# Kernel tuning notes

Hardware: AMD Instinct MI355X
Metric: run time of the kernel (lower is better)

The kernel has to match this reference:

```python
import jax, jax.numpy as jnp
import numpy as np

N_NODES = 50000
N_EDGES = 800000
IN_DIM = 128
HID = 32
HEADS = 4


def _lin_init(key, fan_in, fan_out):
    k1, k2 = jax.random.split(key)
    s = 1.0 / np.sqrt(fan_in)
    W = jax.random.uniform(k1, (fan_in, fan_out), jnp.float32, -s, s)
    b = jax.random.uniform(k2, (fan_out,), jnp.float32, -s, s)
    return W, b


def setup_inputs() -> dict:
    key = jax.random.key(0)
    keys = jax.random.split(key, 12)
    x = jax.random.normal(keys[0], (N_NODES, IN_DIM), jnp.float32)
    edge_index = jax.random.randint(keys[1], (2, N_EDGES), 0, N_NODES, jnp.int64)

    # conv1: in_dim -> heads*hid (128 -> 4*32)
    Wq1, bq1 = _lin_init(keys[2], IN_DIM, HEADS * HID)
    Wk1, bk1 = _lin_init(keys[3], IN_DIM, HEADS * HID)
    Wv1, bv1 = _lin_init(keys[4], IN_DIM, HEADS * HID)
    Ws1, bs1 = _lin_init(keys[5], IN_DIM, HEADS * HID)
    # conv2: 128 -> 1*32
    Wq2, bq2 = _lin_init(keys[6], HEADS * HID, HID)
    Wk2, bk2 = _lin_init(keys[7], HEADS * HID, HID)
    Wv2, bv2 = _lin_init(keys[8], HEADS * HID, HID)
    Ws2, bs2 = _lin_init(keys[9], HEADS * HID, HID)
    # output linear: 32 -> 1
    Wo, bo = _lin_init(keys[10], HID, 1)

    return {
        "x": x, "edge_index": edge_index,
        "Wq1": Wq1, "bq1": bq1, "Wk1": Wk1, "bk1": bk1,
        "Wv1": Wv1, "bv1": bv1, "Ws1": Ws1, "bs1": bs1,
        "Wq2": Wq2, "bq2": bq2, "Wk2": Wk2, "bk2": bk2,
        "Wv2": Wv2, "bv2": bv2, "Ws2": Ws2, "bs2": bs2,
        "Wo": Wo, "bo": bo,
    }


def transformer_conv(x, edge_index, Wq, bq, Wk, bk, Wv, bv, Ws, bs, heads, d):
    # PyG TransformerConv (concat=True, root_weight=True, beta=False, no edge attr).
    n = x.shape[0]
    src, dst = edge_index[0], edge_index[1]  # message j(src) -> i(dst)
    q = (x @ Wq + bq).reshape(n, heads, d)
    k = (x @ Wk + bk).reshape(n, heads, d)
    v = (x @ Wv + bv).reshape(n, heads, d)
    # per-edge attention logits [E, heads]
    logits = (q[dst] * k[src]).sum(-1) / jnp.sqrt(jnp.float32(d))
    # segment softmax over incoming edges of each target node
    m = jax.ops.segment_max(logits, dst, num_segments=n)
    p = jnp.exp(logits - m[dst])
    denom = jax.ops.segment_sum(p, dst, num_segments=n)
    alpha = p / denom[dst]  # [E, heads]
    # weighted scatter-add of values
    msg = alpha[:, :, None] * v[src]  # [E, heads, d]
    aggr = jax.ops.segment_sum(msg, dst, num_segments=n).reshape(n, heads * d)
    return aggr + x @ Ws + bs  # root (skip) connection


def reference(x, edge_index,
              Wq1, bq1, Wk1, bk1, Wv1, bv1, Ws1, bs1,
              Wq2, bq2, Wk2, bk2, Wv2, bv2, Ws2, bs2,
              Wo, bo):
    h = transformer_conv(x, edge_index, Wq1, bq1, Wk1, bk1, Wv1, bv1, Ws1, bs1, HEADS, HID)
    h = jax.nn.relu(h)
    h = transformer_conv(h, edge_index, Wq2, bq2, Wk2, bk2, Wv2, bv2, Ws2, bs2, 1, HID)
    h = jax.nn.relu(h)
    g = h.mean(axis=0)  # [HID]
    return g @ Wo + bo  # [1]
```

## Files before the change

### kernel.cpp

```cpp
#include <hip/hip_runtime.h>
#include <math.h>

#define N_NODES 50000
#define N_EDGES 800000
#define NBK 196
#define BCAP 6144

typedef short short8 __attribute__((ext_vector_type(8)));
typedef float f32x4 __attribute__((ext_vector_type(4)));
typedef float f32x2 __attribute__((ext_vector_type(2)));

__device__ inline unsigned short f2bf(float v) {
  unsigned u = __float_as_uint(v);
  u += 0x7FFFu + ((u >> 16) & 1u);
  return (unsigned short)(u >> 16);
}
__device__ inline float bf2f(unsigned short b) {
  return __uint_as_float(((unsigned)b) << 16);
}
__device__ inline float bflo(unsigned u) { return __uint_as_float(u << 16); }
__device__ inline float bfhi(unsigned u) { return __uint_as_float(u & 0xFFFF0000u); }
__device__ inline unsigned char f2fp8(float v) {
  return (unsigned char)(__builtin_amdgcn_cvt_pk_fp8_f32(v, 0.f, 0, false) & 0xFF);
}
template <bool HI>
__device__ inline f32x2 fp8dec(unsigned u) {
  return __builtin_amdgcn_cvt_pk_f32_fp8(u, HI);
}

#define SCL 0.17677669529663687f

#define CAST_B 6250
#define C1_B 256
#define C2_B 64
__global__ void prep_fused(const float* __restrict__ x,
                           const float* __restrict__ Wq1, const float* __restrict__ Wk1,
                           const float* __restrict__ Wv1, const float* __restrict__ Ws1,
                           const float* __restrict__ bq1, const float* __restrict__ bk1,
                           const float* __restrict__ bv1, const float* __restrict__ bs1,
                           const float* __restrict__ Wq2, const float* __restrict__ Wk2,
                           const float* __restrict__ Wv2, const float* __restrict__ Ws2,
                           const float* __restrict__ bq2, const float* __restrict__ bk2,
                           const float* __restrict__ bv2, const float* __restrict__ bs2,
                           unsigned short* __restrict__ xb, unsigned short* __restrict__ Wt1,
                           float* __restrict__ bcat1, unsigned short* __restrict__ Wt2,
                           float* __restrict__ bcat2, int* __restrict__ bhist,
                           float* __restrict__ ACC) {
  const int b = blockIdx.x, tid = threadIdx.x;
  if (b < CAST_B) {
    int i = b * 256 + tid;
    float4 v = ((const float4*)x)[i];
    ushort4 o;
    o.x = f2bf(v.x); o.y = f2bf(v.y); o.z = f2bf(v.z); o.w = f2bf(v.w);
    ((ushort4*)xb)[i] = o;
  } else if (b < CAST_B + C1_B) {
    int i = (b - CAST_B) * 256 + tid;
    int c = i >> 7, k = i & 127;
    int mi = c >> 7, lc = c & 127;
    const float* W = (mi == 0) ? Wq1 : (mi == 1) ? Wk1 : (mi == 2) ? Wv1 : Ws1;
    float scl = (mi == 0) ? SCL : 1.f;
    Wt1[i] = f2bf(W[(size_t)k * 128 + lc] * scl);
    if (i < 512) {
      int bm = i >> 7, bl = i & 127;
      const float* bb = (bm == 0) ? bq1 : (bm == 1) ? bk1 : (bm == 2) ? bv1 : bs1;
      bcat1[i] = bb[bl] * ((bm == 0) ? SCL : 1.f);
    }
  } else if (b < CAST_B + C1_B + C2_B) {
    int i = (b - CAST_B - C1_B) * 256 + tid;
    int c = i >> 7, k = i & 127;
    int mi = c >> 5, lc = c & 31;
    const float* W = (mi == 0) ? Wq2 : (mi == 1) ? Wk2 : (mi == 2) ? Wv2 : Ws2;
    float scl = (mi == 0) ? SCL : 1.f;
    Wt2[i] = f2bf(W[(size_t)k * 32 + lc] * scl);
    if (i < 128) {
      int bm = i >> 5, bl = i & 31;
      const float* bb = (bm == 0) ? bq2 : (bm == 1) ? bk2 : (bm == 2) ? bv2 : bs2;
      bcat2[i] = bb[bl] * ((bm == 0) ? SCL : 1.f);
    }
  } else {
    if (tid < NBK) bhist[tid] = 0;
    else if (tid >= 224 && tid < 256) ACC[tid - 224] = 0.f;
  }
}

__global__ __launch_bounds__(256) void gemm_conv1(
    const unsigned short* __restrict__ Ab, const unsigned short* __restrict__ Wt,
    const float* __restrict__ bcat, unsigned short* __restrict__ Q1b,
    unsigned short* __restrict__ SK1, unsigned char* __restrict__ KV8, int M) {
  __shared__ __align__(16) unsigned char L[3][64 * 272];
  unsigned short* As = (unsigned short*)L[0];
  const int bm = blockIdx.x * 64;
  const int tid = threadIdx.x, wave = tid >> 6, lane = tid & 63;
  const int lr = lane & 15, q = lane >> 4;

#pragma unroll
  for (int p = 0; p < 4; ++p) {
    int f = tid + p * 256;
    int row = f >> 4, chunk = f & 15;
    int gm = bm + row; if (gm >= M) gm = 0;
    uint4 v = *(const uint4*)(Ab + (size_t)gm * 128 + chunk * 8);
    *(uint4*)&As[row * 136 + chunk * 8] = v;
  }
  __syncthreads();

  const int colbase = wave * 128;
  f32x4 acc[4][8];
#pragma unroll
  for (int i = 0; i < 4; ++i)
#pragma unroll
    for (int j = 0; j < 8; ++j) acc[i][j] = (f32x4){0.f, 0.f, 0.f, 0.f};

#pragma unroll
  for (int ks = 0; ks < 4; ++ks) {
    short8 af[4];
#pragma unroll
    for (int i = 0; i < 4; ++i)
      af[i] = *(short8*)&As[(i * 16 + lr) * 136 + ks * 32 + q * 8];
#pragma unroll
    for (int j = 0; j < 8; ++j) {
      short8 bf = *(const short8*)(Wt + (size_t)(colbase + j * 16 + lr) * 128 + ks * 32 + q * 8);
#pragma unroll
      for (int i = 0; i < 4; ++i)
        acc[i][j] = __builtin_amdgcn_mfma_f32_16x16x32_bf16(af[i], bf, acc[i][j], 0, 0, 0);
    }
  }
  __syncthreads();

  float bj[8];
#pragma unroll
  for (int j = 0; j < 8; ++j) bj[j] = bcat[colbase + j * 16 + lr];

  if (wave == 0 || wave == 3) {
    unsigned short* Ls16 = (unsigned short*)((wave == 0) ? L[1] : L[0]);
#pragma unroll
    for (int i = 0; i < 4; ++i)
#pragma unroll
      for (int r = 0; r < 4; ++r) {
        int row = i * 16 + q * 4 + r;
#pragma unroll
        for (int j = 0; j < 8; ++j)
          Ls16[row * 136 + j * 16 + lr] = f2bf(acc[i][j][r] + bj[j]);
      }
  } else {
    unsigned char* KLs = L[2];
    const int voff = (wave == 2) ? 2 : 0;
#pragma unroll
    for (int i = 0; i < 4; ++i)
#pragma unroll
      for (int r = 0; r < 4; ++r) {
        int row = i * 16 + q * 4 + r;
#pragma unroll
        for (int j = 0; j < 8; ++j) {
          int d = j * 16 + lr;
          KLs[row * 272 + 4 * (d >> 1) + voff + (d & 1)] = f2fp8(acc[i][j][r] + bj[j]);
        }
      }
  }
  __syncthreads();

#pragma unroll
  for (int p = 0; p < 4; ++p) {
    int f = tid + p * 256;
    int row = f >> 4, u = f & 15;
    int gr = bm + row;
    if (gr < M) {
      *(uint4*)(Q1b + (size_t)gr * 128 + u * 8) = *(uint4*)&((unsigned short*)L[1])[row * 136 + u * 8];
      *(uint4*)(KV8 + (size_t)gr * 256 + u * 16) = *(uint4*)&L[2][row * 272 + u * 16];
      *(uint4*)(SK1 + (size_t)gr * 128 + u * 8) = *(uint4*)&((unsigned short*)L[0])[row * 136 + u * 8];
    }
  }
}

__global__ __launch_bounds__(256) void gemm2(
    const unsigned short* __restrict__ Ab, const unsigned short* __restrict__ Wt,
    const float* __restrict__ bcat, unsigned char* __restrict__ C2b, int M) {
  __shared__ __align__(16) unsigned short As[64 * 136];
  __shared__ __align__(16) unsigned char Lsb[64 * 272];
  const int bm = blockIdx.x * 64;
  const int tid = threadIdx.x, wave = tid >> 6, lane = tid & 63;
  const int lr = lane & 15, q = lane >> 4;

#pragma unroll
  for (int p = 0; p < 4; ++p) {
    int f = tid + p * 256;
    int row = f >> 4, chunk = f & 15;
    int gm = bm + row; if (gm >= M) gm = 0;
    uint4 v = *(const uint4*)(Ab + (size_t)gm * 128 + chunk * 8);
    *(uint4*)&As[row * 136 + chunk * 8] = v;
  }
  __syncthreads();

  f32x4 acc[4][2];
#pragma unroll
  for (int i = 0; i < 4; ++i)
#pragma unroll
    for (int j = 0; j < 2; ++j) acc[i][j] = (f32x4){0.f, 0.f, 0.f, 0.f};

#pragma unroll
  for (int ks = 0; ks < 4; ++ks) {
    short8 af[4];
#pragma unroll
    for (int i = 0; i < 4; ++i)
      af[i] = *(short8*)&As[(i * 16 + lr) * 136 + ks * 32 + q * 8];
#pragma unroll
    for (int j = 0; j < 2; ++j) {
      short8 bf = *(const short8*)(Wt + (size_t)(wave * 32 + j * 16 + lr) * 128 + ks * 32 + q * 8);
#pragma unroll
      for (int i = 0; i < 4; ++i)
        acc[i][j] = __builtin_amdgcn_mfma_f32_16x16x32_bf16(af[i], bf, acc[i][j], 0, 0, 0);
    }
  }

  float bj[2];
#pragma unroll
  for (int j = 0; j < 2; ++j) bj[j] = bcat[wave * 32 + j * 16 + lr];
#pragma unroll
  for (int i = 0; i < 4; ++i)
#pragma unroll
    for (int r = 0; r < 4; ++r) {
      int row = i * 16 + q * 4 + r;
#pragma unroll
      for (int j = 0; j < 2; ++j) {
        int c = wave * 32 + j * 16 + lr;
        float val = acc[i][j][r] + bj[j];
        if (c < 32) {
          *(unsigned short*)&Lsb[row * 272 + 2 * c] = f2bf(val);
        } else if (c < 64) {
          int d = c - 32;
          Lsb[row * 272 + 64 + 4 * (d >> 1) + (d & 1)] = f2fp8(val);
        } else if (c < 96) {
          int d = c - 64;
          Lsb[row * 272 + 64 + 4 * (d >> 1) + 2 + (d & 1)] = f2fp8(val);
        } else {
          *(unsigned short*)&Lsb[row * 272 + 192 + 2 * (c - 96)] = f2bf(val);
        }
      }
    }
  __syncthreads();
#pragma unroll
  for (int p = 0; p < 16; ++p) {
    int idx = tid + p * 256;
    int row = idx >> 6, u = idx & 63;
    int gr = bm + row;
    if (gr < M) *(unsigned*)(C2b + (size_t)gr * 256 + u * 4) = *(const unsigned*)&Lsb[row * 272 + u * 4];
  }
}

__global__ void bucket_hist(const int* __restrict__ ei, int* __restrict__ bhist, int E) {
  __shared__ int h[NBK];
  for (int i = threadIdx.x; i < NBK; i += 256) h[i] = 0;
  __syncthreads();
  int e = blockIdx.x * 4096 + threadIdx.x;
#pragma unroll
  for (int p = 0; p < 16; ++p, e += 256)
    if (e < E) atomicAdd(&h[ei[E + e] >> 8], 1);
  __syncthreads();
  for (int i = threadIdx.x; i < NBK; i += 256)
    if (h[i]) atomicAdd(&bhist[i], h[i]);
}

__global__ void bucket_scan(const int* __restrict__ bhist, int* __restrict__ boff,
                            int* __restrict__ bcur) {
  __shared__ int s[256];
  int t = threadIdx.x;
  int v = (t < NBK) ? bhist[t] : 0;
  s[t] = v;
  __syncthreads();
#pragma unroll
  for (int off = 1; off < 256; off <<= 1) {
    int u = (t >= off) ? s[t - off] : 0;
    __syncthreads();
    s[t] += u;
    __syncthreads();
  }
  if (t < NBK) {
    int excl = s[t] - v;
    boff[t] = excl;
    bcur[t] = excl;
  }
  if (t == NBK - 1) boff[NBK] = s[t];
}

__global__ void bucket_scatter(const int* __restrict__ ei, int* __restrict__ bcur,
                               int2* __restrict__ ebuck, int E) {
  __shared__ int lh[NBK];
  for (int i = threadIdx.x; i < NBK; i += 256) lh[i] = 0;
  __syncthreads();
  const int e0 = blockIdx.x * 4096;
  int srcs[16], dsts[16];
#pragma unroll
  for (int p = 0; p < 16; ++p) {
    int e = e0 + p * 256 + threadIdx.x;
    if (e < E) {
      srcs[p] = ei[e];
      dsts[p] = ei[E + e];
      atomicAdd(&lh[dsts[p] >> 8], 1);
    } else dsts[p] = -1;
  }
  __syncthreads();
  for (int i = threadIdx.x; i < NBK; i += 256)
    if (lh[i]) lh[i] = atomicAdd(&bcur[i], lh[i]);
  __syncthreads();
#pragma unroll
  for (int p = 0; p < 16; ++p) {
    if (dsts[p] >= 0) {
      int slot = atomicAdd(&lh[dsts[p] >> 8], 1);
      ebuck[slot] = make_int2(srcs[p], dsts[p]);
    }
  }
}

__global__ void bucket_csr(const int2* __restrict__ ebuck, const int* __restrict__ boff,
                           int* __restrict__ rowptr, int* __restrict__ esrc, int N) {
  const int b = blockIdx.x;
  const int lo = boff[b], hi = boff[b + 1];
  const int cnt = hi - lo;
  __shared__ int hist[256];
  __shared__ int cur[256];
  __shared__ int sorted[BCAP];
  const int t = threadIdx.x;
  hist[t] = 0;
  __syncthreads();
  for (int i = t; i < cnt; i += 256) {
    int2 ed = ebuck[lo + i];
    atomicAdd(&hist[ed.y & 255], 1);
  }
  __syncthreads();
  int v = hist[t];
  sorted[t] = v;
  __syncthreads();
#pragma unroll
  for (int off = 1; off < 256; off <<= 1) {
    int u = (t >= off) ? sorted[t - off] : 0;
    __syncthreads();
    sorted[t] += u;
    __syncthreads();
  }
  int excl = sorted[t] - v;
  cur[t] = excl;
  int node = b * 256 + t;
  if (node <= N) rowptr[node] = lo + excl;
  __syncthreads();
  for (int i = t; i < cnt; i += 256) {
    int2 ed = ebuck[lo + i];
    int slot = atomicAdd(&cur[ed.y & 255], 1);
    if (slot < BCAP) sorted[slot] = ed.x;
    else esrc[lo + slot] = ed.x << 8;
  }
  __syncthreads();
  int lim = cnt < BCAP ? cnt : BCAP;
  for (int i = t; i < lim; i += 256) esrc[lo + i] = sorted[i] << 8;
}

__global__ void node_attn1(const int* __restrict__ rowptr, const int* __restrict__ esrc,
                           const unsigned short* __restrict__ Qb,
                           const unsigned char* __restrict__ KV8,
                           const unsigned short* __restrict__ SK, unsigned short* __restrict__ Hb,
                           int n) {
  int node = (blockIdx.x * blockDim.x + threadIdx.x) >> 6;
  int lane = threadIdx.x & 63;
  if (node >= n) return;
  const int half = lane >> 5, ll = lane & 31;
  const int r0 = rowptr[node], r1 = rowptr[node + 1];
  uint2 qq = *(const uint2*)(Qb + (size_t)node * 128 + ll * 4);
  const float q0 = bflo(qq.x), q1 = bfhi(qq.x), q2 = bflo(qq.y), q3 = bfhi(qq.y);
  float l = 0.f, a0 = 0.f, a1 = 0.f, a2 = 0.f, a3 = 0.f;
  const unsigned char* kvb = KV8 + ll * 8;
  int j = r0;
  for (; j + 8 <= r1; j += 8) {
    int e = j + half * 4;
    int s0 = esrc[e], s1 = esrc[e + 1], s2 = esrc[e + 2], s3 = esrc[e + 3];
    uint2 u0 = *(const uint2*)(kvb + s0);
    uint2 u1 = *(const uint2*)(kvb + s1);
    uint2 u2 = *(const uint2*)(kvb + s2);
    uint2 u3 = *(const uint2*)(kvb + s3);
    f32x2 k0a = fp8dec<false>(u0.x), k0b = fp8dec<false>(u0.y);
    f32x2 k1a = fp8dec<false>(u1.x), k1b = fp8dec<false>(u1.y);
    f32x2 k2a = fp8dec<false>(u2.x), k2b = fp8dec<false>(u2.y);
    f32x2 k3a = fp8dec<false>(u3.x), k3b = fp8dec<false>(u3.y);
    float d0 = q0 * k0a.x + q1 * k0a.y + q2 * k0b.x + q3 * k0b.y;
    float d1 = q0 * k1a.x + q1 * k1a.y + q2 * k1b.x + q3 * k1b.y;
    float d2 = q0 * k2a.x + q1 * k2a.y + q2 * k2b.x + q3 * k2b.y;
    float d3 = q0 * k3a.x + q1 * k3a.y + q2 * k3b.x + q3 * k3b.y;
#pragma unroll
    for (int msk = 1; msk <= 4; msk <<= 1) {
      d0 += __shfl_xor(d0, msk);
      d1 += __shfl_xor(d1, msk);
      d2 += __shfl_xor(d2, msk);
      d3 += __shfl_xor(d3, msk);
    }
    float p0 = __expf(d0), p1 = __expf(d1), p2 = __expf(d2), p3 = __expf(d3);
    l += (p0 + p1) + (p2 + p3);
    f32x2 v0a = fp8dec<true>(u0.x), v0b = fp8dec<true>(u0.y);
    f32x2 v1a = fp8dec<true>(u1.x), v1b = fp8dec<true>(u1.y);
    f32x2 v2a = fp8dec<true>(u2.x), v2b = fp8dec<true>(u2.y);
    f32x2 v3a = fp8dec<true>(u3.x), v3b = fp8dec<true>(u3.y);
    a0 += p0 * v0a.x + p1 * v1a.x + p2 * v2a.x + p3 * v3a.x;
    a1 += p0 * v0a.y + p1 * v1a.y + p2 * v2a.y + p3 * v3a.y;
    a2 += p0 * v0b.x + p1 * v1b.x + p2 * v2b.x + p3 * v3b.x;
    a3 += p0 * v0b.y + p1 * v1b.y + p2 * v2b.y + p3 * v3b.y;
  }
  for (; j < r1; j += 4) {
    int eA = j + half * 2, eB = eA + 1;
    bool vA = eA < r1, vB = eB < r1;
    int sA = esrc[vA ? eA : r0];
    int sB = esrc[vB ? eB : r0];
    uint2 ua = *(const uint2*)(kvb + sA);
    uint2 ub = *(const uint2*)(kvb + sB);
    f32x2 ka1 = fp8dec<false>(ua.x), ka2 = fp8dec<false>(ua.y);
    f32x2 kb1 = fp8dec<false>(ub.x), kb2 = fp8dec<false>(ub.y);
    float dA = q0 * ka1.x + q1 * ka1.y + q2 * ka2.x + q3 * ka2.y;
    float dB = q0 * kb1.x + q1 * kb1.y + q2 * kb2.x + q3 * kb2.y;
#pragma unroll
    for (int msk = 1; msk <= 4; msk <<= 1) {
      dA += __shfl_xor(dA, msk);
      dB += __shfl_xor(dB, msk);
    }
    float pA = vA ? __expf(dA) : 0.f;
    float pB = vB ? __expf(dB) : 0.f;
    l += pA + pB;
    f32x2 va1 = fp8dec<true>(ua.x), va2 = fp8dec<true>(ua.y);
    f32x2 vb1 = fp8dec<true>(ub.x), vb2 = fp8dec<true>(ub.y);
    a0 += pA * va1.x + pB * vb1.x;
    a1 += pA * va1.y + pB * vb1.y;
    a2 += pA * va2.x + pB * vb2.x;
    a3 += pA * va2.y + pB * vb2.y;
  }
  l  += __shfl_xor(l, 32);
  a0 += __shfl_xor(a0, 32);
  a1 += __shfl_xor(a1, 32);
  a2 += __shfl_xor(a2, 32);
  a3 += __shfl_xor(a3, 32);
  float inv = (l > 0.f) ? 1.f / l : 0.f;
  if (half == 0) {
    uint2 sk = *(const uint2*)(SK + (size_t)node * 128 + ll * 4);
    float o0 = fmaxf(bflo(sk.x) + a0 * inv, 0.f);
    float o1 = fmaxf(bfhi(sk.x) + a1 * inv, 0.f);
    float o2 = fmaxf(bflo(sk.y) + a2 * inv, 0.f);
    float o3 = fmaxf(bfhi(sk.y) + a3 * inv, 0.f);
    uint2 hb;
    hb.x = ((unsigned)f2bf(o1) << 16) | (unsigned)f2bf(o0);
    hb.y = ((unsigned)f2bf(o3) << 16) | (unsigned)f2bf(o2);
    *(uint2*)(Hb + (size_t)node * 128 + ll * 4) = hb;
  }
}

__global__ void node_attn2(const int* __restrict__ rowptr, const int* __restrict__ esrc,
                           unsigned char* __restrict__ C2b, int n) {
  int node = (blockIdx.x * blockDim.x + threadIdx.x) >> 6;
  int lane = threadIdx.x & 63;
  if (node >= n) return;
  const int g = lane >> 4, gl = lane & 15;
  const int r0 = rowptr[node], r1 = rowptr[node + 1];
  unsigned qu = *(const unsigned*)(C2b + (size_t)node * 256 + gl * 4);
  const float q0 = bflo(qu), q1 = bfhi(qu);
  float l = 0.f, a0 = 0.f, a1 = 0.f;
  const unsigned char* kvb = C2b + 64 + gl * 4;
  int j = r0;
  for (; j + 8 <= r1; j += 8) {
    int e = j + g * 2;
    int s0 = esrc[e], s1 = esrc[e + 1];
    unsigned u0 = *(const unsigned*)(kvb + s0);
    unsigned u1 = *(const unsigned*)(kvb + s1);
    f32x2 k0 = fp8dec<false>(u0), k1 = fp8dec<false>(u1);
    float d0 = q0 * k0.x + q1 * k0.y;
    float d1 = q0 * k1.x + q1 * k1.y;
#pragma unroll
    for (int msk = 1; msk <= 8; msk <<= 1) {
      d0 += __shfl_xor(d0, msk);
      d1 += __shfl_xor(d1, msk);
    }
    float p0 = __expf(d0), p1 = __expf(d1);
    l += p0 + p1;
    f32x2 v0 = fp8dec<true>(u0), v1 = fp8dec<true>(u1);
    a0 += p0 * v0.x + p1 * v1.x;
    a1 += p0 * v0.y + p1 * v1.y;
  }
  for (; j < r1; j += 4) {
    bool v = (j + g) < r1;
    int s = esrc[v ? j + g : r0];
    unsigned u = *(const unsigned*)(kvb + s);
    f32x2 kd = fp8dec<false>(u);
    float d = q0 * kd.x + q1 * kd.y;
#pragma unroll
    for (int msk = 1; msk <= 8; msk <<= 1) d += __shfl_xor(d, msk);
    float p = v ? __expf(d) : 0.f;
    l += p;
    f32x2 vd = fp8dec<true>(u);
    a0 += p * vd.x;
    a1 += p * vd.y;
  }
#pragma unroll
  for (int msk = 16; msk <= 32; msk <<= 1) {
    l  += __shfl_xor(l, msk);
    a0 += __shfl_xor(a0, msk);
    a1 += __shfl_xor(a1, msk);
  }
  float inv = (l > 0.f) ? 1.f / l : 0.f;
  if (lane < 16) {
    unsigned* h = (unsigned*)(C2b + (size_t)node * 256 + 192 + gl * 4);
    unsigned hu = *h;
    float o0 = bflo(hu) + a0 * inv;
    float o1 = bfhi(hu) + a1 * inv;
    *h = ((unsigned)f2bf(o1) << 16) | (unsigned)f2bf(o0);
  }
}

__global__ void mean_reduce(const unsigned char* __restrict__ C2b, float* __restrict__ ACC, int n) {
  __shared__ float s[256];
  float acc = 0.f;
  int stride = gridDim.x * blockDim.x;
  int total = n * 32;
  for (int i = blockIdx.x * blockDim.x + threadIdx.x; i < total; i += stride) {
    int node = i >> 5, c = i & 31;
    unsigned short h = *(const unsigned short*)(C2b + (size_t)node * 256 + 192 + c * 2);
    acc += fmaxf(bf2f(h), 0.f);
  }
  s[threadIdx.x] = acc;
  __syncthreads();
  for (int off = 128; off >= 32; off >>= 1) {
    if (threadIdx.x < off) s[threadIdx.x] += s[threadIdx.x + off];
    __syncthreads();
  }
  if (threadIdx.x < 32) atomicAdd(&ACC[threadIdx.x], s[threadIdx.x]);
}

__global__ void final_out(const float* __restrict__ ACC, const float* __restrict__ Wo,
                          const float* __restrict__ bo, float* __restrict__ out, float invN) {
  int lane = threadIdx.x;
  float v = 0.f;
  if (lane < 32) v = ACC[lane] * invN * Wo[lane];
  v += __shfl_xor(v, 1);
  v += __shfl_xor(v, 2);
  v += __shfl_xor(v, 4);
  v += __shfl_xor(v, 8);
  v += __shfl_xor(v, 16);
  v += __shfl_xor(v, 32);
  if (lane == 0) out[0] = v + bo[0];
}

extern "C" void kernel_launch(void* const* d_in, const int* in_sizes, int n_in,
                              void* d_out, int out_size, void* d_ws, size_t ws_size,
                              hipStream_t stream) {
  const float* x   = (const float*)d_in[0];
  const int*   ei  = (const int*)d_in[1];
  const float* Wq1 = (const float*)d_in[2];  const float* bq1 = (const float*)d_in[3];
  const float* Wk1 = (const float*)d_in[4];  const float* bk1 = (const float*)d_in[5];
  const float* Wv1 = (const float*)d_in[6];  const float* bv1 = (const float*)d_in[7];
  const float* Ws1 = (const float*)d_in[8];  const float* bs1 = (const float*)d_in[9];
  const float* Wq2 = (const float*)d_in[10]; const float* bq2 = (const float*)d_in[11];
  const float* Wk2 = (const float*)d_in[12]; const float* bk2 = (const float*)d_in[13];
  const float* Wv2 = (const float*)d_in[14]; const float* bv2 = (const float*)d_in[15];
  const float* Ws2 = (const float*)d_in[16]; const float* bs2 = (const float*)d_in[17];
  const float* Wo  = (const float*)d_in[18]; const float* bo  = (const float*)d_in[19];

  char* ws = (char*)d_ws;
  const int N = N_NODES, E = N_EDGES;
  const int GB = (N + 63) / 64;
  const int EB = (E + 4095) / 4096;

  unsigned short* xb  = (unsigned short*)(ws + 0);
  unsigned short* Q1b = (unsigned short*)(ws + 12800000);
  unsigned short* SK1 = (unsigned short*)(ws + 25600000);
  unsigned char*  KV1 = (unsigned char*)(ws + 38400000);
  unsigned short* H1b = (unsigned short*)(ws + 64000000);
  unsigned char*  C2  = (unsigned char*)(ws + 76800000);
  int* rowptr = (int*)(ws + 102400000);
  int* esrc   = (int*)(ws + 102700032);
  int* bhist  = (int*)(ws + 105900032);
  int* boff   = (int*)(ws + 105901056);
  int* bcur   = (int*)(ws + 105902080);
  unsigned short* Wt1   = (unsigned short*)(ws + 105903104);
  unsigned short* Wt2   = (unsigned short*)(ws + 106034176);
  float*          bcat1 = (float*)(ws + 106066944);
  float*          bcat2 = (float*)(ws + 106068992);
  float*          ACC   = (float*)(ws + 106069504);
  int2*           ebuck = (int2*)(ws + 106070016);

  float* out = (float*)d_out;

  dim3 blk(256);

  prep_fused<<<dim3(CAST_B + C1_B + C2_B + 1), blk, 0, stream>>>(
      x, Wq1, Wk1, Wv1, Ws1, bq1, bk1, bv1, bs1,
      Wq2, Wk2, Wv2, Ws2, bq2, bk2, bv2, bs2,
      xb, Wt1, bcat1, Wt2, bcat2, bhist, ACC);

  bucket_hist<<<dim3(EB), blk, 0, stream>>>(ei, bhist, E);
  bucket_scan<<<dim3(1), blk, 0, stream>>>(bhist, boff, bcur);
  bucket_scatter<<<dim3(EB), blk, 0, stream>>>(ei, bcur, ebuck, E);
  bucket_csr<<<dim3(NBK), blk, 0, stream>>>(ebuck, boff, rowptr, esrc, N);

  gemm_conv1<<<dim3(GB), blk, 0, stream>>>(xb, Wt1, bcat1, Q1b, SK1, KV1, N);

  node_attn1<<<dim3((N * 64 + 255) / 256), blk, 0, stream>>>(rowptr, esrc, Q1b, KV1, SK1, H1b, N);

  gemm2<<<dim3(GB), blk, 0, stream>>>(H1b, Wt2, bcat2, C2, N);

  node_attn2<<<dim3((N * 64 + 255) / 256), blk, 0, stream>>>(rowptr, esrc, C2, N);

  mean_reduce<<<dim3(1024), blk, 0, stream>>>(C2, ACC, N);
  final_out<<<dim3(1), dim3(64), 0, stream>>>(ACC, Wo, bo, out, 1.0f / (float)N);
}
```

Measured before the change: 270.4 us.

## Fuse x bf16 cast into conv1 GEMM, merge histogram into prep, pack edges

The standalone fp32-to-bf16 cast of x is removed, and gemm_conv1 now reads fp32 x and converts it while loading into LDS. This avoids writing and re-reading a bf16 copy of x. The bucket histogram is folded into the prep kernel, removing one launch, and zero-initialisation moves to two memset calls. Edge buckets are stored as one packed int (src<<8 | dst&255) instead of int2, halving scatter and CSR traffic. Packing assumes src fits in 24 bits, and the GEMM prologue now reads twice as many bytes per row.

```diff
diff --git a/kernel.cpp b/kernel.cpp
--- a/kernel.cpp
+++ b/kernel.cpp
@@ -30,11 +30,9 @@
 
 #define SCL 0.17677669529663687f
 
-#define CAST_B 6250
-#define C1_B 256
-#define C2_B 64
-__global__ void prep_fused(const float* __restrict__ x,
-                           const float* __restrict__ Wq1, const float* __restrict__ Wk1,
+#define W1_B 256
+#define W2_B 64
+__global__ void prep_fused(const float* __restrict__ Wq1, const float* __restrict__ Wk1,
                            const float* __restrict__ Wv1, const float* __restrict__ Ws1,
                            const float* __restrict__ bq1, const float* __restrict__ bk1,
                            const float* __restrict__ bv1, const float* __restrict__ bs1,
@@ -42,19 +40,12 @@
                            const float* __restrict__ Wv2, const float* __restrict__ Ws2,
                            const float* __restrict__ bq2, const float* __restrict__ bk2,
                            const float* __restrict__ bv2, const float* __restrict__ bs2,
-                           unsigned short* __restrict__ xb, unsigned short* __restrict__ Wt1,
-                           float* __restrict__ bcat1, unsigned short* __restrict__ Wt2,
-                           float* __restrict__ bcat2, int* __restrict__ bhist,
-                           float* __restrict__ ACC) {
+                           unsigned short* __restrict__ Wt1, float* __restrict__ bcat1,
+                           unsigned short* __restrict__ Wt2, float* __restrict__ bcat2,
+                           const int* __restrict__ ei, int* __restrict__ bhist, int E) {
   const int b = blockIdx.x, tid = threadIdx.x;
-  if (b < CAST_B) {
+  if (b < W1_B) {
     int i = b * 256 + tid;
-    float4 v = ((const float4*)x)[i];
-    ushort4 o;
-    o.x = f2bf(v.x); o.y = f2bf(v.y); o.z = f2bf(v.z); o.w = f2bf(v.w);
-    ((ushort4*)xb)[i] = o;
-  } else if (b < CAST_B + C1_B) {
-    int i = (b - CAST_B) * 256 + tid;
     int c = i >> 7, k = i & 127;
     int mi = c >> 7, lc = c & 127;
     const float* W = (mi == 0) ? Wq1 : (mi == 1) ? Wk1 : (mi == 2) ? Wv1 : Ws1;
@@ -65,8 +56,8 @@
       const float* bb = (bm == 0) ? bq1 : (bm == 1) ? bk1 : (bm == 2) ? bv1 : bs1;
       bcat1[i] = bb[bl] * ((bm == 0) ? SCL : 1.f);
     }
-  } else if (b < CAST_B + C1_B + C2_B) {
-    int i = (b - CAST_B - C1_B) * 256 + tid;
+  } else if (b < W1_B + W2_B) {
+    int i = (b - W1_B) * 256 + tid;
     int c = i >> 7, k = i & 127;
     int mi = c >> 5, lc = c & 31;
     const float* W = (mi == 0) ? Wq2 : (mi == 1) ? Wk2 : (mi == 2) ? Wv2 : Ws2;
@@ -78,13 +69,21 @@
       bcat2[i] = bb[bl] * ((bm == 0) ? SCL : 1.f);
     }
   } else {
-    if (tid < NBK) bhist[tid] = 0;
-    else if (tid >= 224 && tid < 256) ACC[tid - 224] = 0.f;
+    __shared__ int h[NBK];
+    for (int i = tid; i < NBK; i += 256) h[i] = 0;
+    __syncthreads();
+    int e = (b - W1_B - W2_B) * 4096 + tid;
+#pragma unroll
+    for (int p = 0; p < 16; ++p, e += 256)
+      if (e < E) atomicAdd(&h[ei[E + e] >> 8], 1);
+    __syncthreads();
+    for (int i = tid; i < NBK; i += 256)
+      if (h[i]) atomicAdd(&bhist[i], h[i]);
   }
 }
 
 __global__ __launch_bounds__(256) void gemm_conv1(
-    const unsigned short* __restrict__ Ab, const unsigned short* __restrict__ Wt,
+    const float* __restrict__ X, const unsigned short* __restrict__ Wt,
     const float* __restrict__ bcat, unsigned short* __restrict__ Q1b,
     unsigned short* __restrict__ SK1, unsigned char* __restrict__ KV8, int M) {
   __shared__ __align__(16) unsigned char L[3][64 * 272];
@@ -94,12 +93,14 @@
   const int lr = lane & 15, q = lane >> 4;
 
 #pragma unroll
-  for (int p = 0; p < 4; ++p) {
+  for (int p = 0; p < 8; ++p) {
     int f = tid + p * 256;
-    int row = f >> 4, chunk = f & 15;
+    int row = f >> 5, c4 = f & 31;
     int gm = bm + row; if (gm >= M) gm = 0;
-    uint4 v = *(const uint4*)(Ab + (size_t)gm * 128 + chunk * 8);
-    *(uint4*)&As[row * 136 + chunk * 8] = v;
+    float4 v = *(const float4*)(X + (size_t)gm * 128 + c4 * 4);
+    ushort4 o;
+    o.x = f2bf(v.x); o.y = f2bf(v.y); o.z = f2bf(v.z); o.w = f2bf(v.w);
+    *(ushort4*)&As[row * 136 + c4 * 4] = o;
   }
   __syncthreads();
 
@@ -246,19 +247,6 @@
   }
 }
 
-__global__ void bucket_hist(const int* __restrict__ ei, int* __restrict__ bhist, int E) {
-  __shared__ int h[NBK];
-  for (int i = threadIdx.x; i < NBK; i += 256) h[i] = 0;
-  __syncthreads();
-  int e = blockIdx.x * 4096 + threadIdx.x;
-#pragma unroll
-  for (int p = 0; p < 16; ++p, e += 256)
-    if (e < E) atomicAdd(&h[ei[E + e] >> 8], 1);
-  __syncthreads();
-  for (int i = threadIdx.x; i < NBK; i += 256)
-    if (h[i]) atomicAdd(&bhist[i], h[i]);
-}
-
 __global__ void bucket_scan(const int* __restrict__ bhist, int* __restrict__ boff,
                             int* __restrict__ bcur) {
   __shared__ int s[256];
@@ -282,20 +270,21 @@
 }
 
 __global__ void bucket_scatter(const int* __restrict__ ei, int* __restrict__ bcur,
-                               int2* __restrict__ ebuck, int E) {
+                               int* __restrict__ ebuck, int E) {
   __shared__ int lh[NBK];
   for (int i = threadIdx.x; i < NBK; i += 256) lh[i] = 0;
   __syncthreads();
   const int e0 = blockIdx.x * 4096;
-  int srcs[16], dsts[16];
+  int pks[16], bks[16];
 #pragma unroll
   for (int p = 0; p < 16; ++p) {
     int e = e0 + p * 256 + threadIdx.x;
     if (e < E) {
-      srcs[p] = ei[e];
-      dsts[p] = ei[E + e];
-      atomicAdd(&lh[dsts[p] >> 8], 1);
-    } else dsts[p] = -1;
+      int src = ei[e], dst = ei[E + e];
+      pks[p] = (src << 8) | (dst & 255);
+      bks[p] = dst >> 8;
+      atomicAdd(&lh[bks[p]], 1);
+    } else bks[p] = -1;
   }
   __syncthreads();
   for (int i = threadIdx.x; i < NBK; i += 256)
@@ -303,14 +292,14 @@
   __syncthreads();
 #pragma unroll
   for (int p = 0; p < 16; ++p) {
-    if (dsts[p] >= 0) {
-      int slot = atomicAdd(&lh[dsts[p] >> 8], 1);
-      ebuck[slot] = make_int2(srcs[p], dsts[p]);
-    }
-  }
-}
-
-__global__ void bucket_csr(const int2* __restrict__ ebuck, const int* __restrict__ boff,
+    if (bks[p] >= 0) {
+      int slot = atomicAdd(&lh[bks[p]], 1);
+      ebuck[slot] = pks[p];
+    }
+  }
+}
+
+__global__ void bucket_csr(const int* __restrict__ ebuck, const int* __restrict__ boff,
                            int* __restrict__ rowptr, int* __restrict__ esrc, int N) {
   const int b = blockIdx.x;
   const int lo = boff[b], hi = boff[b + 1];
@@ -321,10 +310,7 @@
   const int t = threadIdx.x;
   hist[t] = 0;
   __syncthreads();
-  for (int i = t; i < cnt; i += 256) {
-    int2 ed = ebuck[lo + i];
-    atomicAdd(&hist[ed.y & 255], 1);
-  }
+  for (int i = t; i < cnt; i += 256) atomicAdd(&hist[ebuck[lo + i] & 255], 1);
   __syncthreads();
   int v = hist[t];
   sorted[t] = v;
@@ -342,14 +328,14 @@
   if (node <= N) rowptr[node] = lo + excl;
   __syncthreads();
   for (int i = t; i < cnt; i += 256) {
-    int2 ed = ebuck[lo + i];
-    int slot = atomicAdd(&cur[ed.y & 255], 1);
-    if (slot < BCAP) sorted[slot] = ed.x;
-    else esrc[lo + slot] = ed.x << 8;
+    int pk = ebuck[lo + i];
+    int slot = atomicAdd(&cur[pk & 255], 1);
+    if (slot < BCAP) sorted[slot] = pk;
+    else esrc[lo + slot] = pk & 0xFFFFFF00;
   }
   __syncthreads();
   int lim = cnt < BCAP ? cnt : BCAP;
-  for (int i = t; i < lim; i += 256) esrc[lo + i] = sorted[i] << 8;
+  for (int i = t; i < lim; i += 256) esrc[lo + i] = sorted[i] & 0xFFFFFF00;
 }
 
 __global__ void node_attn1(const int* __restrict__ rowptr, const int* __restrict__ esrc,
@@ -559,39 +545,40 @@
   const int GB = (N + 63) / 64;
   const int EB = (E + 4095) / 4096;
 
-  unsigned short* xb  = (unsigned short*)(ws + 0);
-  unsigned short* Q1b = (unsigned short*)(ws + 12800000);
-  unsigned short* SK1 = (unsigned short*)(ws + 25600000);
-  unsigned char*  KV1 = (unsigned char*)(ws + 38400000);
-  unsigned short* H1b = (unsigned short*)(ws + 64000000);
-  unsigned char*  C2  = (unsigned char*)(ws + 76800000);
-  int* rowptr = (int*)(ws + 102400000);
-  int* esrc   = (int*)(ws + 102700032);
-  int* bhist  = (int*)(ws + 105900032);
-  int* boff   = (int*)(ws + 105901056);
-  int* bcur   = (int*)(ws + 105902080);
-  unsigned short* Wt1   = (unsigned short*)(ws + 105903104);
-  unsigned short* Wt2   = (unsigned short*)(ws + 106034176);
-  float*          bcat1 = (float*)(ws + 106066944);
-  float*          bcat2 = (float*)(ws + 106068992);
-  float*          ACC   = (float*)(ws + 106069504);
-  int2*           ebuck = (int2*)(ws + 106070016);
+  unsigned short* Q1b = (unsigned short*)(ws + 0);
+  unsigned short* SK1 = (unsigned short*)(ws + 12800000);
+  unsigned char*  KV1 = (unsigned char*)(ws + 25600000);
+  unsigned short* H1b = (unsigned short*)(ws + 51200000);
+  unsigned char*  C2  = (unsigned char*)(ws + 64000000);
+  int* rowptr = (int*)(ws + 89600000);
+  int* esrc   = (int*)(ws + 89900032);
+  int* bhist  = (int*)(ws + 93100032);
+  int* boff   = (int*)(ws + 93101056);
+  int* bcur   = (int*)(ws + 93102080);
+  unsigned short* Wt1   = (unsigned short*)(ws + 93103104);
+  unsigned short* Wt2   = (unsigned short*)(ws + 93234176);
+  float*          bcat1 = (float*)(ws + 93266944);
+  float*          bcat2 = (float*)(ws + 93268992);
+  float*          ACC   = (float*)(ws + 93269504);
+  int*            ebuck = (int*)(ws + 93270016);
 
   float* out = (float*)d_out;
 
   dim3 blk(256);
 
-  prep_fused<<<dim3(CAST_B + C1_B + C2_B + 1), blk, 0, stream>>>(
-      x, Wq1, Wk1, Wv1, Ws1, bq1, bk1, bv1, bs1,
+  hipMemsetAsync(bhist, 0, NBK * sizeof(int), stream);
+  hipMemsetAsync(ACC, 0, 32 * sizeof(float), stream);
+
+  prep_fused<<<dim3(W1_B + W2_B + EB), blk, 0, stream>>>(
+      Wq1, Wk1, Wv1, Ws1, bq1, bk1, bv1, bs1,
       Wq2, Wk2, Wv2, Ws2, bq2, bk2, bv2, bs2,
-      xb, Wt1, bcat1, Wt2, bcat2, bhist, ACC);
-
-  bucket_hist<<<dim3(EB), blk, 0, stream>>>(ei, bhist, E);
+      Wt1, bcat1, Wt2, bcat2, ei, bhist, E);
+
   bucket_scan<<<dim3(1), blk, 0, stream>>>(bhist, boff, bcur);
   bucket_scatter<<<dim3(EB), blk, 0, stream>>>(ei, bcur, ebuck, E);
   bucket_csr<<<dim3(NBK), blk, 0, stream>>>(ebuck, boff, rowptr, esrc, N);
 
-  gemm_conv1<<<dim3(GB), blk, 0, stream>>>(xb, Wt1, bcat1, Q1b, SK1, KV1, N);
+  gemm_conv1<<<dim3(GB), blk, 0, stream>>>(x, Wt1, bcat1, Q1b, SK1, KV1, N);
 
   node_attn1<<<dim3((N * 64 + 255) / 256), blk, 0, stream>>>(rowptr, esrc, Q1b, KV1, SK1, H1b, N);
 
```

New measurement: 270.0 us. No clear change (-0.2%).
